# Optimization experiments

Measured on AMD Instinct MI355X. Metric: run time of the kernel, lower is better.

Reference implementation:

```python
import jax, jax.numpy as jnp
import numpy as np

# Longformer-base-4096 config (layers reduced 12->4 for CPU tractability)
B_, S_, DM, H_, DH, L_, FF, V = 1, 4096, 768, 12, 64, 4, 3072, 50265
BLOCK = 256  # one-sided window; total attention window = 512


def layer_norm(x, g, b, eps=1e-5):
    m = jnp.mean(x, axis=-1, keepdims=True)
    v = jnp.mean(jnp.square(x - m), axis=-1, keepdims=True)
    return (x - m) * jax.lax.rsqrt(v + eps) * g + b


def sliding_attention(q, k, v, key_mask):
    """Banded local attention: each query attends keys within +/- BLOCK positions.
    q,k,v: (B,H,S,Dh); key_mask: (B,S) 1 for valid tokens."""
    B, H, S, D = q.shape
    nb = S // BLOCK
    qb = q.reshape(B, H, nb, BLOCK, D)
    kp = jnp.pad(k, ((0, 0), (0, 0), (BLOCK, BLOCK), (0, 0)))
    vp = jnp.pad(v, ((0, 0), (0, 0), (BLOCK, BLOCK), (0, 0)))
    # each query block n sees key blocks n-1, n, n+1  -> window of 3*BLOCK keys
    idx = jnp.arange(nb)[:, None] * BLOCK + jnp.arange(3 * BLOCK)[None, :]  # (nb, 3B)
    kw = kp[:, :, idx]  # (B,H,nb,3B,D)
    vw = vp[:, :, idx]
    scores = jnp.einsum('bhnqd,bhnkd->bhnqk', qb, kw) / np.float32(np.sqrt(D))
    # relative position of key w.r.t. query inside the 3-block window
    rel = jnp.arange(3 * BLOCK)[None, :] - BLOCK - jnp.arange(BLOCK)[:, None]  # (BLOCK,3B)
    band = (jnp.abs(rel) <= BLOCK)[None, None, None]  # (1,1,1,BLOCK,3B)
    mp = jnp.pad(key_mask.astype(bool), ((0, 0), (BLOCK, BLOCK)))
    mw = mp[:, idx][:, None, :, None, :]  # (B,1,nb,1,3B)
    scores = jnp.where(band & mw, scores, -1e9)
    probs = jax.nn.softmax(scores, axis=-1)
    out = jnp.einsum('bhnqk,bhnkd->bhnqd', probs, vw)
    return out.reshape(B, H, S, D)


def encode(ids, mask, word_emb, pos_emb, emb_g, emb_b, layers):
    B, S = ids.shape
    x = word_emb[ids] + pos_emb[None, :S]
    x = layer_norm(x, emb_g, emb_b)

    def step(x, p):
        wq, bq, wk, bk, wv, bv, wo, bo, g1, b1, w1, c1, w2, c2, g2, b2 = p
        heads = lambda y: y.reshape(B, S, H_, DH).transpose(0, 2, 1, 3)
        q = heads(x @ wq + bq)
        k = heads(x @ wk + bk)
        vv = heads(x @ wv + bv)
        a = sliding_attention(q, k, vv, mask)
        a = a.transpose(0, 2, 1, 3).reshape(B, S, DM) @ wo + bo
        x2 = layer_norm(x + a, g1, b1)  # post-LN (RoBERTa/Longformer)
        h = jax.nn.gelu(x2 @ w1 + c1)
        x3 = layer_norm(x2 + h @ w2 + c2, g2, b2)
        return x3, None

    x, _ = jax.lax.scan(jax.checkpoint(step), x, layers)
    return x


def setup_inputs() -> dict:
    key = jax.random.key(0)
    ks = jax.random.split(key, 16)
    s = 0.02
    d = {
        'input_ids1': jax.random.randint(ks[0], (B_, S_), 0, V),
        'input_ids2': jax.random.randint(ks[1], (B_, S_), 0, V),
        'attention_mask1': jnp.ones((B_, S_), dtype=jnp.int32),
        'attention_mask2': jnp.ones((B_, S_), dtype=jnp.int32),
        'word_emb': jax.random.normal(ks[2], (V, DM)) * s,
        'pos_emb': jax.random.normal(ks[3], (S_, DM)) * s,
        'emb_g': jnp.ones((DM,)), 'emb_b': jnp.zeros((DM,)),
        'wq': jax.random.normal(ks[4], (L_, DM, DM)) * s, 'bq': jnp.zeros((L_, DM)),
        'wk': jax.random.normal(ks[5], (L_, DM, DM)) * s, 'bk': jnp.zeros((L_, DM)),
        'wv': jax.random.normal(ks[6], (L_, DM, DM)) * s, 'bv': jnp.zeros((L_, DM)),
        'wo': jax.random.normal(ks[7], (L_, DM, DM)) * s, 'bo': jnp.zeros((L_, DM)),
        'ln1_g': jnp.ones((L_, DM)), 'ln1_b': jnp.zeros((L_, DM)),
        'w_ff1': jax.random.normal(ks[8], (L_, DM, FF)) * s, 'b_ff1': jnp.zeros((L_, FF)),
        'w_ff2': jax.random.normal(ks[9], (L_, FF, DM)) * s, 'b_ff2': jnp.zeros((L_, DM)),
        'ln2_g': jnp.ones((L_, DM)), 'ln2_b': jnp.zeros((L_, DM)),
        'dense_w': jax.random.normal(ks[10], (DM, 1)) * s, 'dense_b': jnp.zeros((1,)),
    }
    return d


def reference(input_ids1, input_ids2, attention_mask1, attention_mask2,
              word_emb, pos_emb, emb_g, emb_b,
              wq, bq, wk, bk, wv, bv, wo, bo,
              ln1_g, ln1_b, w_ff1, b_ff1, w_ff2, b_ff2, ln2_g, ln2_b,
              dense_w, dense_b):
    layers = (wq, bq, wk, bk, wv, bv, wo, bo, ln1_g, ln1_b,
              w_ff1, b_ff1, w_ff2, b_ff2, ln2_g, ln2_b)
    o1 = encode(input_ids1, attention_mask1, word_emb, pos_emb, emb_g, emb_b, layers)
    o2 = encode(input_ids2, attention_mask2, word_emb, pos_emb, emb_g, emb_b, layers)
    diff = o1.mean(1, keepdims=True) - o2.mean(1, keepdims=True)  # (B,1,DM)
    return jax.nn.sigmoid(diff @ dense_w + dense_b)  # (B,1,1)
```

## Files before the change

### kernel.cpp

```cpp
#include <hip/hip_runtime.h>

typedef __bf16 bf16_t;
typedef bf16_t bf16x8 __attribute__((ext_vector_type(8)));
typedef float f32x4 __attribute__((ext_vector_type(4)));
typedef unsigned short u16x4 __attribute__((ext_vector_type(4)));
typedef unsigned short u16x8 __attribute__((ext_vector_type(8)));
typedef float f32x4v __attribute__((ext_vector_type(4)));

#define NL 4

__device__ __forceinline__ float bf2f(unsigned short u){
  unsigned int x = ((unsigned int)u) << 16;
  return __builtin_bit_cast(float, x);
}
__device__ __forceinline__ unsigned short f2bf(float f){
  unsigned int u = __builtin_bit_cast(unsigned int, f);
  u += 0x7FFFu + ((u >> 16) & 1u);
  return (unsigned short)(u >> 16);
}
__device__ __forceinline__ void gload16(const void* g, void* l){
  __builtin_amdgcn_global_load_lds((const __attribute__((address_space(1))) unsigned int*)g,
                                   (__attribute__((address_space(3))) unsigned int*)l, 16, 0, 0);
}

__global__ __launch_bounds__(256) void transpose_cvt(const float* __restrict__ src,
                                                     unsigned short* __restrict__ dst,
                                                     int R, int C){
  __shared__ unsigned short tile[64][72];
  size_t boff = (size_t)blockIdx.z * (size_t)R * (size_t)C;
  int tc0 = blockIdx.x * 64, tr0 = blockIdx.y * 64;
  int t = threadIdx.x;
  int r = t >> 2, cs = (t & 3) * 16;
  const float* s = src + boff + (size_t)(tr0 + r) * C + tc0 + cs;
  #pragma unroll
  for (int j = 0; j < 16; j += 4){
    f32x4v v = *(const f32x4v*)(s + j);
    #pragma unroll
    for (int q = 0; q < 4; q++) tile[r][cs + j + q] = f2bf(v[q]);
  }
  __syncthreads();
  int n = t >> 2;
  unsigned short* d = dst + boff + (size_t)(tc0 + n) * R + tr0 + cs;
  u16x8 o0, o1;
  #pragma unroll
  for (int j = 0; j < 8; j++){ o0[j] = tile[cs + j][n]; o1[j] = tile[cs + 8 + j][n]; }
  *(u16x8*)d       = o0;
  *(u16x8*)(d + 8) = o1;
}

__global__ __launch_bounds__(256) void transpose64(const unsigned short* __restrict__ src,
                                                   unsigned short* __restrict__ dst,
                                                   int R, int C){
  __shared__ unsigned short tile[64][72];
  size_t boff = (size_t)blockIdx.z * (size_t)R * (size_t)C;
  int tc0 = blockIdx.x * 64, tr0 = blockIdx.y * 64;
  int t = threadIdx.x;
  int r = t >> 2, cs = (t & 3) * 16;
  const unsigned short* s = src + boff + (size_t)(tr0 + r) * C + tc0 + cs;
  *(u16x8*)(&tile[r][cs])     = *(const u16x8*)(s);
  *(u16x8*)(&tile[r][cs + 8]) = *(const u16x8*)(s + 8);
  __syncthreads();
  int n = t >> 2;
  unsigned short* d = dst + boff + (size_t)(tc0 + n) * R + tr0 + cs;
  u16x8 o0, o1;
  #pragma unroll
  for (int j = 0; j < 8; j++){ o0[j] = tile[cs + j][n]; o1[j] = tile[cs + 8 + j][n]; }
  *(u16x8*)d       = o0;
  *(u16x8*)(d + 8) = o1;
}

template<int ACT>
__device__ __forceinline__ void gemm_core(const unsigned short* __restrict__ A,
                                          const unsigned short* __restrict__ BT,
                                          const float* __restrict__ bias,
                                          unsigned short* __restrict__ C,
                                          int m0, int n0, int N, int K){
  __shared__ unsigned short lds[24576];
  const int t = threadIdx.x;
  const int lane = t & 63;
  const int l15 = lane & 15, l4 = lane >> 4;
  const int w = t >> 6, wm = w >> 1, wn = w & 1;
  f32x4 acc[4][4] = {};
  const int rowA = t >> 2;
  const int segA = ((t & 3) ^ ((t >> 3) & 3)) * 8;
  const unsigned short* Abase = A  + (size_t)(m0 + rowA) * K + segA;
  const unsigned short* Bbase = BT + (size_t)(n0 + rowA) * K + segA;
  const int rslot = (l4 ^ ((l15 >> 1) & 3)) * 8;

  auto STAGE = [&](int k0, int buf){
    unsigned short* As_ = lds + buf * 8192;
    unsigned short* Bs_ = As_ + 4096;
    gload16(Abase + k0,                  As_ + t * 8);
    gload16(Abase + (size_t)64 * K + k0, As_ + 2048 + t * 8);
    gload16(Bbase + k0,                  Bs_ + t * 8);
    gload16(Bbase + (size_t)64 * K + k0, Bs_ + 2048 + t * 8);
  };
  auto COMPUTE = [&](int buf){
    const unsigned short* Ab = lds + buf * 8192;
    const unsigned short* Bb = Ab + 4096;
    bf16x8 af[4], bfr[4];
    #pragma unroll
    for (int i = 0; i < 4; i++){
      af[i]  = *(const bf16x8*)(Ab + (wm * 64 + i * 16 + l15) * 32 + rslot);
      bfr[i] = *(const bf16x8*)(Bb + (wn * 64 + i * 16 + l15) * 32 + rslot);
    }
    #pragma unroll
    for (int j = 0; j < 4; j++)
      #pragma unroll
      for (int i = 0; i < 4; i++)
        acc[j][i] = __builtin_amdgcn_mfma_f32_16x16x32_bf16(bfr[j], af[i], acc[j][i], 0, 0, 0);
  };

  const int NK = K >> 5;
  STAGE(0, 0); STAGE(32, 1); STAGE(64, 2);
  int buf = 0;
  for (int k = 0; k < NK - 3; k++){
    asm volatile("s_waitcnt vmcnt(8)" ::: "memory");
    __builtin_amdgcn_s_barrier();
    __builtin_amdgcn_sched_barrier(0);
    COMPUTE(buf);
    __builtin_amdgcn_sched_barrier(0);
    __builtin_amdgcn_s_barrier();
    STAGE((k + 3) << 5, buf);
    buf = buf == 2 ? 0 : buf + 1;
  }
  asm volatile("s_waitcnt vmcnt(8)" ::: "memory");
  __builtin_amdgcn_s_barrier();
  __builtin_amdgcn_sched_barrier(0);
  COMPUTE(buf);
  buf = buf == 2 ? 0 : buf + 1;
  asm volatile("s_waitcnt vmcnt(4)" ::: "memory");
  __builtin_amdgcn_s_barrier();
  __builtin_amdgcn_sched_barrier(0);
  COMPUTE(buf);
  buf = buf == 2 ? 0 : buf + 1;
  asm volatile("s_waitcnt vmcnt(0)" ::: "memory");
  __builtin_amdgcn_s_barrier();
  __builtin_amdgcn_sched_barrier(0);
  COMPUTE(buf);

  const int mB = m0 + wm * 64;
  const int nB = n0 + wn * 64;
  #pragma unroll
  for (int i = 0; i < 4; i++){
    unsigned short* crow = C + (size_t)(mB + i * 16 + l15) * N + nB;
    #pragma unroll
    for (int j = 0; j < 4; j++){
      const int nn = j * 16 + l4 * 4;
      f32x4v bb = *(const f32x4v*)(bias + nB + nn);
      u16x4 pk;
      #pragma unroll
      for (int r = 0; r < 4; r++){
        float v = acc[j][i][r] + bb[r];
        if (ACT == 1){
          float e = __expf(-1.5957691216057308f * (v + 0.044715f * v * v * v));
          v = __fdividef(v, 1.0f + e);
        }
        pk[r] = f2bf(v);
      }
      *(u16x4*)(crow + nn) = pk;
    }
  }
}

template<int ACT>
__global__ __launch_bounds__(256) void gemm_bt(const unsigned short* __restrict__ A,
                                               const unsigned short* __restrict__ BT,
                                               const float* __restrict__ bias,
                                               unsigned short* __restrict__ C, int N, int K){
  const int b = blockIdx.x;
  const int s = b >> 3;
  const int m = (b & 7) * 8 + (s & 7);
  const int n = s >> 3;
  gemm_core<ACT>(A, BT, bias, C, m * 128, n * 128, N, K);
}

__global__ __launch_bounds__(256) void qkv_gemm(const unsigned short* __restrict__ A,
                                                const unsigned short* __restrict__ wT,
                                                int l,
                                                const float* __restrict__ bq,
                                                const float* __restrict__ bk,
                                                const float* __restrict__ bv,
                                                unsigned short* __restrict__ q,
                                                unsigned short* __restrict__ k,
                                                unsigned short* __restrict__ v){
  const int b = blockIdx.x;
  const int s = b >> 3;
  const int m0 = ((b & 7) * 8 + (s & 7)) * 128;
  const int grp = s >> 3;
  const int sel = grp / 6, col = grp % 6;
  const unsigned short* BT = wT + ((size_t)sel * NL + l) * (size_t)(768 * 768);
  const float* bias = sel == 0 ? bq : (sel == 1 ? bk : bv);
  unsigned short* C = sel == 0 ? q : (sel == 1 ? k : v);
  gemm_core<0>(A, BT, bias, C, m0, col * 128, 768, 768);
}

__global__ __launch_bounds__(256, 4) void attn_kernel(const unsigned short* __restrict__ Q,
                                                      const unsigned short* __restrict__ Km,
                                                      const unsigned short* __restrict__ VT,
                                                      const int* __restrict__ mask1,
                                                      const int* __restrict__ mask2,
                                                      unsigned short* __restrict__ O){
  const int qt = blockIdx.x, h = blockIdx.y, seq = blockIdx.z;
  const int t = threadIdx.x, lane = t & 63, w = t >> 6;
  const int l15 = lane & 15, l4 = lane >> 4;
  __shared__ unsigned short Kc[64 * 64];
  __shared__ unsigned short VTc[64 * 64];
  __shared__ unsigned short Ps[4][16 * 64];
  const unsigned short* Qp  = Q  + (size_t)seq * 4096 * 768;
  const unsigned short* Kp  = Km + (size_t)seq * 4096 * 768;
  const unsigned short* VTp = VT + (size_t)seq * 768 * 4096;
  const int* mask = seq ? mask2 : mask1;
  unsigned short* Op = O + (size_t)seq * 4096 * 768;

  const int q0 = qt * 64 + w * 16;
  const int qg = q0 + l15;
  const int swz = (l15 & 7) * 8;

  bf16x8 qf[2];
  #pragma unroll
  for (int ks = 0; ks < 2; ks++)
    qf[ks] = *(const bf16x8*)(Qp + (size_t)qg * 768 + h * 64 + ks * 32 + l4 * 8);

  f32x4 oacc[4] = {};
  float rm = -1e30f, rl = 0.0f;

  const int kstart = qt * 64 >= 256 ? qt * 64 - 256 : 0;
  const int kend0  = qt * 64 + 320;
  const int kend   = kend0 > 4096 ? 4096 : kend0;
  unsigned short* psw = &Ps[w][0];

  const int rr = t >> 3;
  const int c8 = (((t & 7) ^ (rr & 7)) * 8);

  for (int kb = kstart; kb < kend; kb += 64){
    gload16(Kp  + (size_t)(kb + rr) * 768 + h * 64 + c8,       Kc + t * 8);
    gload16(Kp  + (size_t)(kb + 32 + rr) * 768 + h * 64 + c8,  Kc + 2048 + t * 8);
    gload16(VTp + (size_t)(h * 64 + rr) * 4096 + kb + c8,      VTc + t * 8);
    gload16(VTp + (size_t)(h * 64 + 32 + rr) * 4096 + kb + c8, VTc + 2048 + t * 8);
    __syncthreads();
    if (kb + 63 >= q0 - 256 && kb <= q0 + 271){
      f32x4 sT[4];
      #pragma unroll
      for (int mt = 0; mt < 4; mt++){
        const unsigned short* kr = Kc + (mt * 16 + l15) * 64;
        bf16x8 kf0 = *(const bf16x8*)(kr + ((l4 * 8) ^ swz));
        bf16x8 kf1 = *(const bf16x8*)(kr + ((32 + l4 * 8) ^ swz));
        f32x4 z = {};
        z      = __builtin_amdgcn_mfma_f32_16x16x32_bf16(kf0, qf[0], z, 0, 0, 0);
        sT[mt] = __builtin_amdgcn_mfma_f32_16x16x32_bf16(kf1, qf[1], z, 0, 0, 0);
      }
      float smax = -1e30f;
      #pragma unroll
      for (int mt = 0; mt < 4; mt++){
        int4 mv = *(const int4*)(mask + kb + mt * 16 + l4 * 4);
        #pragma unroll
        for (int r = 0; r < 4; r++){
          int kgl = kb + mt * 16 + l4 * 4 + r;
          int d = kgl - qg;
          int mvv = (r == 0) ? mv.x : (r == 1) ? mv.y : (r == 2) ? mv.z : mv.w;
          bool ok = (mvv != 0) && (d <= 256) && (d >= -256);
          float v = sT[mt][r] * 0.125f;
          sT[mt][r] = ok ? v : -1e30f;
          smax = fmaxf(smax, sT[mt][r]);
        }
      }
      smax = fmaxf(smax, __shfl_xor(smax, 16, 64));
      smax = fmaxf(smax, __shfl_xor(smax, 32, 64));
      float nm = fmaxf(rm, smax);
      float sc = __expf(rm - nm);
      rm = nm;
      float psum = 0.0f;
      #pragma unroll
      for (int mt = 0; mt < 4; mt++){
        u16x4 pk;
        #pragma unroll
        for (int r = 0; r < 4; r++){
          float p = (sT[mt][r] > -1e29f) ? __expf(sT[mt][r] - nm) : 0.0f;
          psum += p;
          pk[r] = f2bf(p);
        }
        *(u16x4*)(psw + l15 * 64 + ((mt * 16 + l4 * 4) ^ swz)) = pk;
      }
      psum += __shfl_xor(psum, 16, 64);
      psum += __shfl_xor(psum, 32, 64);
      rl = rl * sc + psum;
      float scq[4];
      #pragma unroll
      for (int r = 0; r < 4; r++) scq[r] = __shfl(sc, l4 * 4 + r, 64);
      #pragma unroll
      for (int g = 0; g < 4; g++)
        #pragma unroll
        for (int r = 0; r < 4; r++) oacc[g][r] *= scq[r];
      asm volatile("s_waitcnt lgkmcnt(0)" ::: "memory");
      __builtin_amdgcn_sched_barrier(0);
      bf16x8 pa0 = *(const bf16x8*)(psw + l15 * 64 + ((l4 * 8) ^ swz));
      bf16x8 pa1 = *(const bf16x8*)(psw + l15 * 64 + ((32 + l4 * 8) ^ swz));
      #pragma unroll
      for (int g = 0; g < 4; g++){
        const unsigned short* vr = VTc + (g * 16 + l15) * 64;
        bf16x8 vb0 = *(const bf16x8*)(vr + ((l4 * 8) ^ swz));
        bf16x8 vb1 = *(const bf16x8*)(vr + ((32 + l4 * 8) ^ swz));
        oacc[g] = __builtin_amdgcn_mfma_f32_16x16x32_bf16(pa0, vb0, oacc[g], 0, 0, 0);
        oacc[g] = __builtin_amdgcn_mfma_f32_16x16x32_bf16(pa1, vb1, oacc[g], 0, 0, 0);
      }
    }
    __syncthreads();
  }
  float rlq[4];
  #pragma unroll
  for (int r = 0; r < 4; r++) rlq[r] = __shfl(rl, l4 * 4 + r, 64);
  #pragma unroll
  for (int g = 0; g < 4; g++)
    #pragma unroll
    for (int r = 0; r < 4; r++){
      float v = oacc[g][r] / rlq[r];
      Op[(size_t)(q0 + l4 * 4 + r) * 768 + h * 64 + g * 16 + l15] = f2bf(v);
    }
}

__global__ __launch_bounds__(192) void embed_ln(const int* __restrict__ ids1,
                                                const int* __restrict__ ids2,
                                                const float* __restrict__ we,
                                                const float* __restrict__ pe,
                                                const float* __restrict__ g,
                                                const float* __restrict__ b,
                                                unsigned short* __restrict__ out){
  const int row = blockIdx.x;
  const int seq = row >> 12, s = row & 4095;
  const int t = threadIdx.x;
  const int id = (seq ? ids2 : ids1)[s];
  f32x4v wvv = *(const f32x4v*)(we + (size_t)id * 768 + t * 4);
  f32x4v pv  = *(const f32x4v*)(pe + (size_t)s * 768 + t * 4);
  float v[4];
  #pragma unroll
  for (int j = 0; j < 4; j++) v[j] = wvv[j] + pv[j];
  float sum = 0, ss = 0;
  #pragma unroll
  for (int j = 0; j < 4; j++){ sum += v[j]; ss += v[j] * v[j]; }
  for (int off = 1; off < 64; off <<= 1){ sum += __shfl_xor(sum, off, 64); ss += __shfl_xor(ss, off, 64); }
  __shared__ float red[2][3];
  int wid = t >> 6;
  if ((t & 63) == 0){ red[0][wid] = sum; red[1][wid] = ss; }
  __syncthreads();
  sum = red[0][0] + red[0][1] + red[0][2];
  ss  = red[1][0] + red[1][1] + red[1][2];
  float mean = sum * (1.0f / 768.0f);
  float var  = ss * (1.0f / 768.0f) - mean * mean;
  float rstd = rsqrtf(var + 1e-5f);
  f32x4v gv = *(const f32x4v*)(g + t * 4);
  f32x4v bv = *(const f32x4v*)(b + t * 4);
  u16x4 o;
  #pragma unroll
  for (int j = 0; j < 4; j++) o[j] = f2bf((v[j] - mean) * rstd * gv[j] + bv[j]);
  *(u16x4*)(out + (size_t)row * 768 + t * 4) = o;
}

__global__ __launch_bounds__(192) void add_ln(const unsigned short* __restrict__ A,
                                              const unsigned short* __restrict__ Bp,
                                              const float* __restrict__ g,
                                              const float* __restrict__ b,
                                              unsigned short* __restrict__ out){
  const int row = blockIdx.x;
  const int t = threadIdx.x;
  u16x4 a4 = *(const u16x4*)(A  + (size_t)row * 768 + t * 4);
  u16x4 b4 = *(const u16x4*)(Bp + (size_t)row * 768 + t * 4);
  float v[4];
  #pragma unroll
  for (int j = 0; j < 4; j++) v[j] = bf2f(a4[j]) + bf2f(b4[j]);
  float sum = 0, ss = 0;
  #pragma unroll
  for (int j = 0; j < 4; j++){ sum += v[j]; ss += v[j] * v[j]; }
  for (int off = 1; off < 64; off <<= 1){ sum += __shfl_xor(sum, off, 64); ss += __shfl_xor(ss, off, 64); }
  __shared__ float red[2][3];
  int wid = t >> 6;
  if ((t & 63) == 0){ red[0][wid] = sum; red[1][wid] = ss; }
  __syncthreads();
  sum = red[0][0] + red[0][1] + red[0][2];
  ss  = red[1][0] + red[1][1] + red[1][2];
  float mean = sum * (1.0f / 768.0f);
  float var  = ss * (1.0f / 768.0f) - mean * mean;
  float rstd = rsqrtf(var + 1e-5f);
  f32x4v gv = *(const f32x4v*)(g + t * 4);
  f32x4v bv = *(const f32x4v*)(b + t * 4);
  u16x4 o;
  #pragma unroll
  for (int j = 0; j < 4; j++) o[j] = f2bf((v[j] - mean) * rstd * gv[j] + bv[j]);
  *(u16x4*)(out + (size_t)row * 768 + t * 4) = o;
}

__global__ __launch_bounds__(256) void colmean(const unsigned short* __restrict__ X,
                                               float* __restrict__ mean){
  const int t = threadIdx.x;
  const int seq = blockIdx.y;
  const int r0 = blockIdx.x * 64;
  const unsigned short* base = X + ((size_t)seq * 4096 + r0) * 768;
  float a0 = 0, a1 = 0, a2 = 0;
  for (int r = 0; r < 64; r++){
    const unsigned short* p = base + (size_t)r * 768;
    a0 += bf2f(p[t]);
    a1 += bf2f(p[t + 256]);
    a2 += bf2f(p[t + 512]);
  }
  atomicAdd(&mean[seq * 768 + t], a0);
  atomicAdd(&mean[seq * 768 + t + 256], a1);
  atomicAdd(&mean[seq * 768 + t + 512], a2);
}

__global__ __launch_bounds__(256) void final_k(const float* __restrict__ means,
                                               const float* __restrict__ dw,
                                               const float* __restrict__ db,
                                               float* __restrict__ out){
  const int t = threadIdx.x;
  float part = 0;
  for (int c = t; c < 768; c += 256)
    part += (means[c] - means[768 + c]) * (1.0f / 4096.0f) * dw[c];
  for (int off = 1; off < 64; off <<= 1) part += __shfl_xor(part, off, 64);
  __shared__ float red[4];
  if ((t & 63) == 0) red[t >> 6] = part;
  __syncthreads();
  if (t == 0){
    float r = red[0] + red[1] + red[2] + red[3] + db[0];
    out[0] = 1.0f / (1.0f + expf(-r));
  }
}

__global__ void sentinel_k(float* out){ out[0] = -1.0f; }

extern "C" void kernel_launch(void* const* d_in, const int* in_sizes, int n_in,
                              void* d_out, int out_size, void* d_ws, size_t ws_size,
                              hipStream_t stream){
  (void)in_sizes; (void)n_in; (void)out_size;
  const int* ids1  = (const int*)d_in[0];
  const int* ids2  = (const int*)d_in[1];
  const int* mask1 = (const int*)d_in[2];
  const int* mask2 = (const int*)d_in[3];
  const float* we = (const float*)d_in[4];
  const float* pe = (const float*)d_in[5];
  const float* eg = (const float*)d_in[6];
  const float* eb = (const float*)d_in[7];
  const float* wq = (const float*)d_in[8];
  const float* bq = (const float*)d_in[9];
  const float* wk = (const float*)d_in[10];
  const float* bk = (const float*)d_in[11];
  const float* wv = (const float*)d_in[12];
  const float* bv = (const float*)d_in[13];
  const float* wo = (const float*)d_in[14];
  const float* bo = (const float*)d_in[15];
  const float* g1 = (const float*)d_in[16];
  const float* b1 = (const float*)d_in[17];
  const float* w1 = (const float*)d_in[18];
  const float* c1 = (const float*)d_in[19];
  const float* w2 = (const float*)d_in[20];
  const float* c2 = (const float*)d_in[21];
  const float* g2 = (const float*)d_in[22];
  const float* b2 = (const float*)d_in[23];
  const float* dw = (const float*)d_in[24];
  const float* db = (const float*)d_in[25];
  float* outp = (float*)d_out;

  char* ws = (char*)d_ws;
  size_t off = 0;
  auto alloc = [&](size_t bytes) -> char* {
    char* p = ws + off;
    off += (bytes + 255) & ~(size_t)255;
    return p;
  };
  const size_t W768 = (size_t)768 * 768;
  const size_t WFF  = (size_t)768 * 3072;
  unsigned short* wqkvT = (unsigned short*)alloc(3 * NL * W768 * 2);
  unsigned short* woT   = (unsigned short*)alloc(NL * W768 * 2);
  unsigned short* w1T   = (unsigned short*)alloc(NL * WFF * 2);
  unsigned short* w2T   = (unsigned short*)alloc(NL * WFF * 2);
  unsigned short* xb    = (unsigned short*)alloc((size_t)8192 * 768 * 2);
  unsigned short* qb_   = (unsigned short*)alloc((size_t)8192 * 768 * 2);
  unsigned short* kb_   = (unsigned short*)alloc((size_t)8192 * 768 * 2);
  unsigned short* vb_   = (unsigned short*)alloc((size_t)8192 * 768 * 2);
  unsigned short* hb    = (unsigned short*)alloc((size_t)8192 * 3072 * 2);
  unsigned short* vt    = (unsigned short*)alloc((size_t)2 * 768 * 4096 * 2);
  float* means          = (float*)alloc(2 * 768 * 4);
  if (off > ws_size){ sentinel_k<<<1, 1, 0, stream>>>(outp); return; }

  transpose_cvt<<<dim3(12, 12, NL), 256, 0, stream>>>(wq, wqkvT,                 768, 768);
  transpose_cvt<<<dim3(12, 12, NL), 256, 0, stream>>>(wk, wqkvT + NL * W768,     768, 768);
  transpose_cvt<<<dim3(12, 12, NL), 256, 0, stream>>>(wv, wqkvT + 2 * NL * W768, 768, 768);
  transpose_cvt<<<dim3(12, 12, NL), 256, 0, stream>>>(wo, woT,                   768, 768);
  transpose_cvt<<<dim3(48, 12, NL), 256, 0, stream>>>(w1, w1T,                   768, 3072);
  transpose_cvt<<<dim3(12, 48, NL), 256, 0, stream>>>(w2, w2T,                   3072, 768);

  embed_ln<<<8192, 192, 0, stream>>>(ids1, ids2, we, pe, eg, eb, xb);

  for (int l = 0; l < NL; l++){
    qkv_gemm<<<1152, 256, 0, stream>>>(xb, wqkvT, l, bq + l * 768, bk + l * 768, bv + l * 768,
                                       qb_, kb_, vb_);
    transpose64<<<dim3(12, 64, 2), 256, 0, stream>>>(vb_, vt, 4096, 768);
    attn_kernel<<<dim3(64, 12, 2), 256, 0, stream>>>(qb_, kb_, vt, mask1, mask2, vb_);
    gemm_bt<0><<<384, 256, 0, stream>>>(vb_, woT + (size_t)l * W768, bo + l * 768, qb_, 768, 768);
    add_ln<<<8192, 192, 0, stream>>>(xb, qb_, g1 + l * 768, b1 + l * 768, kb_);
    gemm_bt<1><<<1536, 256, 0, stream>>>(kb_, w1T + (size_t)l * WFF, c1 + l * 3072, hb, 3072, 768);
    gemm_bt<0><<<384, 256, 0, stream>>>(hb, w2T + (size_t)l * WFF, c2 + l * 768, vb_, 768, 3072);
    add_ln<<<8192, 192, 0, stream>>>(kb_, vb_, g2 + l * 768, b2 + l * 768, xb);
  }

  hipMemsetAsync(means, 0, 2 * 768 * 4, stream);
  colmean<<<dim3(64, 2), 256, 0, stream>>>(xb, means);
  final_k<<<1, 256, 0, stream>>>(means, dw, db, outp);
}
```

Before: 1.084 ms.

## Use BK=64 double-buffered K tiles with 8-way XOR swizzle in GEMM core

Changes the GEMM main loop from a triple-buffered K=32 tile pipeline to a double-buffered K=64 pipeline. Each stage now loads 8 async 16-byte chunks per thread, and compute runs two MFMA k-substeps per barrier pair, with the LDS swizzle widened to 8 slots to fit the 64-element rows. The aim is to halve the number of barriers and loop iterations per GEMM and amortize sync overhead. In exchange, LDS use grows to 64KB per block, which may lower occupancy, and prefetch depth drops from three stages to two.

```diff
diff --git a/kernel.cpp b/kernel.cpp
--- a/kernel.cpp
+++ b/kernel.cpp
@@ -75,69 +75,71 @@
                                           const float* __restrict__ bias,
                                           unsigned short* __restrict__ C,
                                           int m0, int n0, int N, int K){
-  __shared__ unsigned short lds[24576];
+  __shared__ unsigned short lds[32768];
   const int t = threadIdx.x;
   const int lane = t & 63;
   const int l15 = lane & 15, l4 = lane >> 4;
   const int w = t >> 6, wm = w >> 1, wn = w & 1;
   f32x4 acc[4][4] = {};
-  const int rowA = t >> 2;
-  const int segA = ((t & 3) ^ ((t >> 3) & 3)) * 8;
-  const unsigned short* Abase = A  + (size_t)(m0 + rowA) * K + segA;
-  const unsigned short* Bbase = BT + (size_t)(n0 + rowA) * K + segA;
-  const int rslot = (l4 ^ ((l15 >> 1) & 3)) * 8;
+  const int rr = t >> 3;
+  const int c8 = ((t & 7) ^ (rr & 7)) * 8;
+  const unsigned short* Abase = A  + (size_t)(m0 + rr) * K + c8;
+  const unsigned short* Bbase = BT + (size_t)(n0 + rr) * K + c8;
 
   auto STAGE = [&](int k0, int buf){
-    unsigned short* As_ = lds + buf * 8192;
-    unsigned short* Bs_ = As_ + 4096;
-    gload16(Abase + k0,                  As_ + t * 8);
-    gload16(Abase + (size_t)64 * K + k0, As_ + 2048 + t * 8);
-    gload16(Bbase + k0,                  Bs_ + t * 8);
-    gload16(Bbase + (size_t)64 * K + k0, Bs_ + 2048 + t * 8);
+    unsigned short* As_ = lds + buf * 16384;
+    unsigned short* Bs_ = As_ + 8192;
+    #pragma unroll
+    for (int it = 0; it < 4; it++){
+      gload16(Abase + (size_t)(it * 32) * K + k0, As_ + (it * 256 + t) * 8);
+      gload16(Bbase + (size_t)(it * 32) * K + k0, Bs_ + (it * 256 + t) * 8);
+    }
   };
   auto COMPUTE = [&](int buf){
-    const unsigned short* Ab = lds + buf * 8192;
-    const unsigned short* Bb = Ab + 4096;
-    bf16x8 af[4], bfr[4];
+    const unsigned short* Ab = lds + buf * 16384;
+    const unsigned short* Bb = Ab + 8192;
     #pragma unroll
-    for (int i = 0; i < 4; i++){
-      af[i]  = *(const bf16x8*)(Ab + (wm * 64 + i * 16 + l15) * 32 + rslot);
-      bfr[i] = *(const bf16x8*)(Bb + (wn * 64 + i * 16 + l15) * 32 + rslot);
+    for (int kk = 0; kk < 2; kk++){
+      bf16x8 af[4], bfr[4];
+      const int cs = kk * 4;
+      #pragma unroll
+      for (int i = 0; i < 4; i++){
+        const int ra = wm * 64 + i * 16 + l15;
+        const int rb = wn * 64 + i * 16 + l15;
+        const int so = ((cs + l4) ^ (l15 & 7)) * 8;
+        af[i]  = *(const bf16x8*)(Ab + ra * 64 + so);
+        bfr[i] = *(const bf16x8*)(Bb + rb * 64 + so);
+      }
+      #pragma unroll
+      for (int j = 0; j < 4; j++)
+        #pragma unroll
+        for (int i = 0; i < 4; i++)
+          acc[j][i] = __builtin_amdgcn_mfma_f32_16x16x32_bf16(bfr[j], af[i], acc[j][i], 0, 0, 0);
     }
-    #pragma unroll
-    for (int j = 0; j < 4; j++)
-      #pragma unroll
-      for (int i = 0; i < 4; i++)
-        acc[j][i] = __builtin_amdgcn_mfma_f32_16x16x32_bf16(bfr[j], af[i], acc[j][i], 0, 0, 0);
   };
 
-  const int NK = K >> 5;
-  STAGE(0, 0); STAGE(32, 1); STAGE(64, 2);
-  int buf = 0;
-  for (int k = 0; k < NK - 3; k++){
+  const int S = K >> 6;
+  STAGE(0, 0); STAGE(64, 1);
+  int cur = 0;
+  for (int k = 0; k < S - 2; k++){
     asm volatile("s_waitcnt vmcnt(8)" ::: "memory");
     __builtin_amdgcn_s_barrier();
     __builtin_amdgcn_sched_barrier(0);
-    COMPUTE(buf);
+    COMPUTE(cur);
     __builtin_amdgcn_sched_barrier(0);
     __builtin_amdgcn_s_barrier();
-    STAGE((k + 3) << 5, buf);
-    buf = buf == 2 ? 0 : buf + 1;
+    STAGE((k + 2) << 6, cur);
+    cur ^= 1;
   }
   asm volatile("s_waitcnt vmcnt(8)" ::: "memory");
   __builtin_amdgcn_s_barrier();
   __builtin_amdgcn_sched_barrier(0);
-  COMPUTE(buf);
-  buf = buf == 2 ? 0 : buf + 1;
-  asm volatile("s_waitcnt vmcnt(4)" ::: "memory");
-  __builtin_amdgcn_s_barrier();
-  __builtin_amdgcn_sched_barrier(0);
-  COMPUTE(buf);
-  buf = buf == 2 ? 0 : buf + 1;
+  COMPUTE(cur);
+  cur ^= 1;
   asm volatile("s_waitcnt vmcnt(0)" ::: "memory");
   __builtin_amdgcn_s_barrier();
   __builtin_amdgcn_sched_barrier(0);
-  COMPUTE(buf);
+  COMPUTE(cur);
 
   const int mB = m0 + wm * 64;
   const int nB = n0 + wn * 64;
```

Result: faster. 1.025 ms (-5.5%).
